# Optimization experiments

Measured on AMD Instinct MI355X. Metric: run time of the kernel, lower is better.

## Reference

```python
import jax, jax.numpy as jnp
import numpy as np

N_GRAPHS = 16
NPG = 420               # nodes per graph (fc1 expects 420*64 flatten)
N = N_GRAPHS * NPG      # 6720
DEG = 8
E = N * DEG             # 53760
HEADS = 4
IN_DIM = 2048
C1 = 1024               # per-head channels, layer 1
C2 = 64                 # layer 2 channels
OUT_DIM = 18
SLOPE = 0.2             # GATConv leaky_relu negative_slope


def _seg_softmax(scores, idx, n):
    # numerically-stable softmax over edges grouped by destination node
    m = jax.lax.stop_gradient(jax.ops.segment_max(scores, idx, num_segments=n))
    ex = jnp.exp(scores - m[idx])
    den = jax.ops.segment_sum(ex, idx, num_segments=n)
    return ex / (den[idx] + 1e-16)


def _transformer_conv(x, src, dst, wq, bq, wk, bk, wv, bv, ws, bs, heads, ch):
    # PyG TransformerConv defaults: concat=True, beta=False, root_weight=True, dropout=0
    n = x.shape[0]
    q = (x @ wq + bq).reshape(n, heads, ch)
    k = (x @ wk + bk).reshape(n, heads, ch)
    v = (x @ wv + bv).reshape(n, heads, ch)
    alpha = jnp.einsum('ehc,ehc->eh', q[dst], k[src]) / (ch ** 0.5)  # [E,H]
    alpha = _seg_softmax(alpha, dst, n)
    out = jax.ops.segment_sum(v[src] * alpha[..., None], dst, num_segments=n)  # [N,H,C]
    return out.reshape(n, heads * ch) + (x @ ws + bs)  # skip connection (lin_skip)


def _gat_conv(x, src, dst, w, a_src, a_dst, bias, heads, ch, concat):
    # PyG GATConv defaults: add_self_loops=True, negative_slope=0.2, lin has no bias
    n = x.shape[0]
    loop = jnp.arange(n, dtype=src.dtype)
    s = jnp.concatenate([src, loop])
    d = jnp.concatenate([dst, loop])
    h = (x @ w).reshape(n, heads, ch)
    es = jnp.einsum('nhc,hc->nh', h, a_src)
    ed = jnp.einsum('nhc,hc->nh', h, a_dst)
    e = jax.nn.leaky_relu(es[s] + ed[d], SLOPE)  # [E+N, H]
    alpha = _seg_softmax(e, d, n)
    out = jax.ops.segment_sum(h[s] * alpha[..., None], d, num_segments=n)  # [N,H,C]
    out = out.reshape(n, heads * ch) if concat else out.mean(axis=1)
    return out + bias


def setup_inputs() -> dict:
    key = jax.random.key(0)
    it = iter(jax.random.split(key, 64))
    def nrm(shape, scale):
        return jax.random.normal(next(it), shape, jnp.float32) * scale
    def lin(fi, fo):
        return nrm((fi, fo), float(1.0 / np.sqrt(fi)))
    p = {}
    p['x'] = nrm((N, IN_DIM), 1.0)
    p['edge_index'] = jax.random.randint(next(it), (2, E), 0, N, dtype=jnp.int32)
    for nm in ['t1_wq', 't1_wk', 't1_wv', 't1_ws']:
        p[nm] = lin(IN_DIM, HEADS * C1)
    for nm in ['t1_bq', 't1_bk', 't1_bv', 't1_bs']:
        p[nm] = jnp.zeros((HEADS * C1,), jnp.float32)
    # TransformerConv 2: 4096 -> 64, 1 head
    for nm in ['t2_wq', 't2_wk', 't2_wv', 't2_ws']:
        p[nm] = lin(HEADS * C1, C2)
    for nm in ['t2_bq', 't2_bk', 't2_bv', 't2_bs']:
        p[nm] = jnp.zeros((C2,), jnp.float32)
    p['g1_w'] = lin(IN_DIM, HEADS * C1)
    p['g1_as'] = nrm((HEADS, C1), 0.02)
    p['g1_ad'] = nrm((HEADS, C1), 0.02)
    p['g1_b'] = jnp.zeros((HEADS * C1,), jnp.float32)
    # GATConv 2: 4096 -> 64, 1 head, concat=False (mean)
    p['g2_w'] = lin(HEADS * C1, C2)
    p['g2_as'] = nrm((1, C2), 0.02)
    p['g2_ad'] = nrm((1, C2), 0.02)
    p['g2_b'] = jnp.zeros((C2,), jnp.float32)
    # MLP head
    p['fc1_w'] = lin(NPG * C2, 256); p['fc1_b'] = jnp.zeros((256,), jnp.float32)
    p['fc2_w'] = lin(256, 128);      p['fc2_b'] = jnp.zeros((128,), jnp.float32)
    p['fc3_w'] = lin(128, 64);       p['fc3_b'] = jnp.zeros((64,), jnp.float32)
    p['fc4_w'] = lin(64, OUT_DIM);   p['fc4_b'] = jnp.zeros((OUT_DIM,), jnp.float32)
    return p


def _forward(edge_index, x,
             t1_wq, t1_bq, t1_wk, t1_bk, t1_wv, t1_bv, t1_ws, t1_bs,
             t2_wq, t2_bq, t2_wk, t2_bk, t2_wv, t2_bv, t2_ws, t2_bs,
             g1_w, g1_as, g1_ad, g1_b, g2_w, g2_as, g2_ad, g2_b,
             fc1_w, fc1_b, fc2_w, fc2_b, fc3_w, fc3_b, fc4_w, fc4_b):
    src, dst = edge_index[0], edge_index[1]
    h = jax.nn.relu(_transformer_conv(x, src, dst, t1_wq, t1_bq, t1_wk, t1_bk,
                                      t1_wv, t1_bv, t1_ws, t1_bs, HEADS, C1))
    h = jax.nn.relu(_transformer_conv(h, src, dst, t2_wq, t2_bq, t2_wk, t2_bk,
                                      t2_wv, t2_bv, t2_ws, t2_bs, 1, C2))
    z = jax.nn.relu(_gat_conv(x, src, dst, g1_w, g1_as, g1_ad, g1_b, HEADS, C1, True))
    z = jax.nn.relu(_gat_conv(z, src, dst, g2_w, g2_as, g2_ad, g2_b, 1, C2, False))
    s = (h + z).reshape(-1, NPG * C2)          # [n_graphs, 26880]
    s = jax.nn.relu(s @ fc1_w + fc1_b)          # dropout = identity at eval
    s = jax.nn.relu(s @ fc2_w + fc2_b)
    s = jax.nn.relu(s @ fc3_w + fc3_b)
    return s @ fc4_w + fc4_b                    # [n_graphs, OUT_DIM]


def reference(x, edge_index,
              t1_wq, t1_bq, t1_wk, t1_bk, t1_wv, t1_bv, t1_ws, t1_bs,
              t2_wq, t2_bq, t2_wk, t2_bk, t2_wv, t2_bv, t2_ws, t2_bs,
              g1_w, g1_as, g1_ad, g1_b, g2_w, g2_as, g2_ad, g2_b,
              fc1_w, fc1_b, fc2_w, fc2_b, fc3_w, fc3_b, fc4_w, fc4_b):
    return _forward(edge_index, x,
                    t1_wq, t1_bq, t1_wk, t1_bk, t1_wv, t1_bv, t1_ws, t1_bs,
                    t2_wq, t2_bq, t2_wk, t2_bk, t2_wv, t2_bv, t2_ws, t2_bs,
                    g1_w, g1_as, g1_ad, g1_b, g2_w, g2_as, g2_ad, g2_b,
                    fc1_w, fc1_b, fc2_w, fc2_b, fc3_w, fc3_b, fc4_w, fc4_b)
```

## Files before the change

kernel.cpp:

```cpp
#include <hip/hip_runtime.h>
#include <stdint.h>
#include <stdio.h>

#define NNODES 6720
#define NEDGES 53760
#define NGRAPH 16
#define INDIM  2048
#define HEADS1 4
#define C1DIM  1024
#define D1     4096
#define C2DIM  64
#define N2     320
#define OUTDIM 18

typedef unsigned short u16;
typedef unsigned int   u32;

__device__ __forceinline__ float b2f(u16 u) {
  union { float f; u32 u; } v; v.u = ((u32)u) << 16; return v.f;
}
__device__ __forceinline__ u16 f2b(float f) {
  union { float f; u32 u; } v; v.f = f;
  u32 r = v.u + 0x7FFFu + ((v.u >> 16) & 1u);
  return (u16)(r >> 16);
}
__device__ __forceinline__ float ldf(const void* p, long i, int isf) {
  return isf ? ((const float*)p)[i] : b2f(((const u16*)p)[i]);
}

typedef __attribute__((ext_vector_type(8))) short bf16x8;
typedef __attribute__((ext_vector_type(4))) float f32x4;

__device__ __forceinline__ void gld_lds16(const u16* g, u16* l) {
  __builtin_amdgcn_global_load_lds((const __attribute__((address_space(1))) void*)g,
                                   (__attribute__((address_space(3))) void*)l, 16, 0, 0);
}

__global__ void detect_dtype(const u16* __restrict__ x, int* flag) {
  __shared__ int cnt;
  if (threadIdx.x == 0) cnt = 0;
  __syncthreads();
  int c = 0;
  for (int i = threadIdx.x; i < 4096; i += 256) {
    u16 u = x[2 * i];
    int e = (u >> 7) & 0xFF;
    if (e >= 118 && e <= 135) c++;
  }
  atomicAdd(&cnt, c);
  __syncthreads();
  if (threadIdx.x == 0) *flag = (cnt > 2048) ? 0 : 1;
}

__global__ void conv_any(const void* __restrict__ src, u16* __restrict__ dst,
                         long n, const int* __restrict__ flag) {
  long i = (long)blockIdx.x * 256 + threadIdx.x;
  long stride = (long)gridDim.x * 256;
  int isf = *flag;
  if (isf) {
    const float* s = (const float*)src;
    for (long j = i; j < n; j += stride) dst[j] = f2b(s[j]);
  } else {
    const u16* s = (const u16*)src;
    for (long j = i; j < n; j += stride) dst[j] = s[j];
  }
}

#define NSMALL 13
struct SmallConv {
  const void* src[NSMALL];
  u16*        dst[NSMALL];
  int         n[NSMALL];
};
__global__ void conv_small(SmallConv sc, const int* __restrict__ flag) {
  int b = blockIdx.x;
  int isf = *flag;
  const void* s = sc.src[b];
  u16* d = sc.dst[b];
  int n = sc.n[b];
  if (isf) {
    const float* sf = (const float*)s;
    for (int i = threadIdx.x; i < n; i += 256) d[i] = f2b(sf[i]);
  } else {
    const u16* sb = (const u16*)s;
    for (int i = threadIdx.x; i < n; i += 256) d[i] = sb[i];
  }
}

__global__ __launch_bounds__(256) void transpose_any(const void* __restrict__ src,
                                                     u16* __restrict__ dst,
                                                     int K, int Ncols,
                                                     const int* __restrict__ flag) {
  __shared__ u16 tile[32][33];
  int isf = *flag;
  int tx = threadIdx.x & 31, ty = threadIdx.x >> 5;
  int c0 = blockIdx.x * 32, r0 = blockIdx.y * 32;
  if (isf) {
    const float* s = (const float*)src;
    #pragma unroll
    for (int i = 0; i < 32; i += 8)
      tile[ty + i][tx] = f2b(s[(long)(r0 + ty + i) * Ncols + c0 + tx]);
  } else {
    const u16* s = (const u16*)src;
    #pragma unroll
    for (int i = 0; i < 32; i += 8)
      tile[ty + i][tx] = s[(long)(r0 + ty + i) * Ncols + c0 + tx];
  }
  __syncthreads();
  #pragma unroll
  for (int i = 0; i < 32; i += 8)
    dst[(long)(c0 + ty + i) * K + r0 + tx] = tile[tx][ty + i];
}

__global__ void pack_bias(const void* bq1, const void* bk1, const void* bv1, const void* bs1,
                          const void* bq2, const void* bk2, const void* bv2, const void* bs2,
                          float* bias1, float* bias2, const int* flag) {
  int isf = *flag;
  int i = blockIdx.x * 256 + threadIdx.x;
  if (i < 20480) {
    float v = 0.f;
    if (i < 4096) v = ldf(bq1, i, isf);
    else if (i < 8192)  v = ldf(bk1, i - 4096, isf);
    else if (i < 12288) v = ldf(bv1, i - 8192, isf);
    else if (i < 16384) v = ldf(bs1, i - 12288, isf);
    bias1[i] = v;
  } else if (i < 20480 + N2) {
    int j = i - 20480; float v = 0.f;
    if (j < 64) v = ldf(bq2, j, isf);
    else if (j < 128) v = ldf(bk2, j - 64, isf);
    else if (j < 192) v = ldf(bv2, j - 128, isf);
    else if (j < 256) v = ldf(bs2, j - 192, isf);
    bias2[j] = v;
  }
}

__global__ __launch_bounds__(256) void gemm_bt_r3(const u16* __restrict__ A,
                                                  const u16* __restrict__ BT,
                                                  const float* __restrict__ bias,
                                                  u16* __restrict__ C,
                                                  int M, int N, int K) {
  __shared__ u16 As[3][128 * 32];
  __shared__ u16 Bs[3][128 * 32];

  const int tid = threadIdx.x, lane = tid & 63, wave = tid >> 6;
  const int m0 = blockIdx.y * 128, n0 = blockIdx.x * 128;
  const int wm = (wave >> 1) * 64, wn = (wave & 1) * 64;

  const int srow = tid >> 2, scp = tid & 3;
  const int scl8 = (scp ^ ((srow >> 1) & 3)) * 8;
  int ar0 = m0 + srow;      if (ar0 >= M) ar0 = M - 1;
  int ar1 = m0 + srow + 64; if (ar1 >= M) ar1 = M - 1;
  const u16* ag0 = A + (long)ar0 * K + scl8;
  const u16* ag1 = A + (long)ar1 * K + scl8;
  const u16* bg0 = BT + (long)(n0 + srow) * K + scl8;
  const u16* bg1 = BT + (long)(n0 + srow + 64) * K + scl8;

  f32x4 acc[4][4];
  #pragma unroll
  for (int i = 0; i < 4; i++)
    #pragma unroll
    for (int j = 0; j < 4; j++) { f32x4 z = {0.f, 0.f, 0.f, 0.f}; acc[i][j] = z; }

  const int fr = lane & 15, q = lane >> 4;
  const int fq = (q ^ ((fr >> 1) & 3)) * 8;
  const int aoff = (wm + fr) * 32 + fq;
  const int boff = (wn + fr) * 32 + fq;

  const int NT = K >> 5;

  auto STAGE = [&](int t, int b) {
    const long k0 = (long)t * 32;
    gld_lds16(ag0 + k0, &As[b][(size_t)tid * 8]);
    gld_lds16(ag1 + k0, &As[b][2048 + (size_t)tid * 8]);
    gld_lds16(bg0 + k0, &Bs[b][(size_t)tid * 8]);
    gld_lds16(bg1 + k0, &Bs[b][2048 + (size_t)tid * 8]);
  };

  STAGE(0, 0); STAGE(1, 1);

  int cur = 0, nxt = 2;
  for (int t = 0; t < NT; ++t) {
    if (t < NT - 1) {
      asm volatile("s_waitcnt vmcnt(4)\n\ts_barrier" ::: "memory");
    } else {
      asm volatile("s_waitcnt vmcnt(0)\n\ts_barrier" ::: "memory");
    }
    if (t + 2 < NT) STAGE(t + 2, nxt);

    const u16* ab = &As[cur][0];
    const u16* bb = &Bs[cur][0];
    bf16x8 af[4], bfv[4];
    #pragma unroll
    for (int i = 0; i < 4; i++) af[i]  = *(const bf16x8*)(ab + aoff + i * 512);
    #pragma unroll
    for (int j = 0; j < 4; j++) bfv[j] = *(const bf16x8*)(bb + boff + j * 512);

    #pragma unroll
    for (int i = 0; i < 4; i++)
      #pragma unroll
      for (int j = 0; j < 4; j++)
        acc[i][j] = __builtin_amdgcn_mfma_f32_16x16x32_bf16(af[i], bfv[j], acc[i][j], 0, 0, 0);

    cur = (cur == 2) ? 0 : cur + 1;
    nxt = (nxt == 2) ? 0 : nxt + 1;
  }

  const int q4 = (lane >> 4) * 4, cl = lane & 15;
  #pragma unroll
  for (int i = 0; i < 4; i++)
    #pragma unroll
    for (int r = 0; r < 4; r++) {
      int row = m0 + wm + i * 16 + q4 + r;
      if (row < M) {
        #pragma unroll
        for (int j = 0; j < 4; j++) {
          int col = n0 + wn + j * 16 + cl;
          C[(long)row * N + col] = f2b(acc[i][j][r] + bias[col]);
        }
      }
    }
}

__global__ __launch_bounds__(256) void gemm2_64(const u16* __restrict__ h1,
                                                const u16* __restrict__ z1,
                                                const u16* __restrict__ wt2,
                                                const float* __restrict__ bias2,
                                                u16* __restrict__ y2) {
  __shared__ u16 As[64 * 64];
  __shared__ u16 Bs[64 * 64];
  const int nt = blockIdx.x;
  const u16* A = (nt < 4) ? h1 : z1;
  const u16* BT = wt2 + (size_t)nt * 64 * D1;
  const int m0 = blockIdx.y * 64, n0 = nt * 64;
  const int tid = threadIdx.x, lane = tid & 63, wave = tid >> 6;

  const int sr = tid >> 3, cp = tid & 7;
  const int cgl8 = (cp ^ (sr & 7)) * 8;
  const u16* ag0 = A + (long)(m0 + sr) * D1 + cgl8;
  const u16* ag1 = ag0 + (long)32 * D1;
  const u16* bg0 = BT + (long)sr * D1 + cgl8;
  const u16* bg1 = bg0 + (long)32 * D1;
  u16* al0 = As + tid * 8;  u16* al1 = As + 2048 + tid * 8;
  u16* bl0 = Bs + tid * 8;  u16* bl1 = Bs + 2048 + tid * 8;

  f32x4 acc[4];
  #pragma unroll
  for (int j = 0; j < 4; j++) { f32x4 z = {0.f, 0.f, 0.f, 0.f}; acc[j] = z; }

  const int fr = lane & 15, q = lane >> 4;
  const int x0 = ((q)     ^ (fr & 7)) * 8;
  const int x1 = ((4 + q) ^ (fr & 7)) * 8;
  const u16* apA = As + (wave * 16 + fr) * 64;

  for (int k0 = 0; k0 < D1; k0 += 64) {
    __syncthreads();
    gld_lds16(ag0 + k0, al0);
    gld_lds16(ag1 + k0, al1);
    gld_lds16(bg0 + k0, bl0);
    gld_lds16(bg1 + k0, bl1);
    __syncthreads();
    bf16x8 a0 = *(const bf16x8*)(apA + x0);
    bf16x8 a1 = *(const bf16x8*)(apA + x1);
    #pragma unroll
    for (int j = 0; j < 4; j++) {
      bf16x8 b0 = *(const bf16x8*)(Bs + (j * 16 + fr) * 64 + x0);
      acc[j] = __builtin_amdgcn_mfma_f32_16x16x32_bf16(a0, b0, acc[j], 0, 0, 0);
    }
    #pragma unroll
    for (int j = 0; j < 4; j++) {
      bf16x8 b1 = *(const bf16x8*)(Bs + (j * 16 + fr) * 64 + x1);
      acc[j] = __builtin_amdgcn_mfma_f32_16x16x32_bf16(a1, b1, acc[j], 0, 0, 0);
    }
  }
  const int q4 = (lane >> 4) * 4, cl = lane & 15;
  #pragma unroll
  for (int j = 0; j < 4; j++)
    #pragma unroll
    for (int r = 0; r < 4; r++) {
      int row = m0 + wave * 16 + q4 + r;
      int col = n0 + j * 16 + cl;
      y2[(long)row * N2 + col] = f2b(acc[j][r] + bias2[col]);
    }
}

__global__ void zero_kernel(int* deg, float* f1sum) {
  int i = blockIdx.x * 256 + threadIdx.x;
  if (i < NNODES) deg[i] = 0;
  if (i < NGRAPH * 256) f1sum[i] = 0.f;
}

__global__ void count_deg(const int* __restrict__ ei, int* deg) {
  int e = blockIdx.x * 256 + threadIdx.x;
  if (e < NEDGES) atomicAdd(&deg[ei[NEDGES + e]], 1);
}

__global__ __launch_bounds__(1024) void scan_deg(const int* __restrict__ deg, int* off, int* cur) {
  __shared__ int sh[1024];
  const int t = threadIdx.x;
  const int PER = 7;
  int base = t * PER;
  int loc[PER];
  int sum = 0;
  #pragma unroll
  for (int i = 0; i < PER; i++) {
    int v = (base + i < NNODES) ? deg[base + i] : 0;
    loc[i] = sum; sum += v;
  }
  sh[t] = sum;
  __syncthreads();
  for (int d = 1; d < 1024; d <<= 1) {
    int v = (t >= d) ? sh[t - d] : 0;
    __syncthreads();
    sh[t] += v;
    __syncthreads();
  }
  int prev = (t > 0) ? sh[t - 1] : 0;
  #pragma unroll
  for (int i = 0; i < PER; i++) {
    int idx = base + i;
    if (idx <= NNODES) {
      int v = prev + loc[i];
      off[idx] = v;
      if (idx < NNODES) cur[idx] = v;
    }
  }
}

__global__ void scatter_edges(const int* __restrict__ ei, int* cur,
                              int* esrc, int* edst) {
  int e = blockIdx.x * 256 + threadIdx.x;
  if (e < NEDGES) {
    int s = ei[e], d = ei[NEDGES + e];
    int p = atomicAdd(&cur[d], 1);
    esrc[p] = s; edst[p] = d;
  }
}

__global__ __launch_bounds__(256) void t1_score_csr(const u16* __restrict__ yqk,
                                                    const int* __restrict__ off,
                                                    const int* __restrict__ esrc,
                                                    float* __restrict__ sc) {
  __shared__ float qsh[4096];
  int n = blockIdx.x, tid = threadIdx.x, lane = tid & 63, wave = tid >> 6;
  const u16* qr = yqk + (long)n * 8192;
  for (int i = tid * 8; i < 4096; i += 2048) {
    uint4 qa = *(const uint4*)(qr + i);
    const u16* qs = (const u16*)&qa;
    #pragma unroll
    for (int j = 0; j < 8; j++) qsh[i + j] = b2f(qs[j]);
  }
  __syncthreads();
  int p0 = off[n], p1 = off[n + 1];
  for (int p = p0 + wave; p < p1; p += 4) {
    const u16* k = yqk + (long)esrc[p] * 8192 + 4096;
    float dot[HEADS1];
    #pragma unroll
    for (int h = 0; h < HEADS1; h++) dot[h] = 0.f;
    #pragma unroll
    for (int h = 0; h < HEADS1; h++) {
      #pragma unroll
      for (int c = 0; c < 2; c++) {
        int idx = h * C1DIM + c * 512 + lane * 8;
        uint4 ka = *(const uint4*)(k + idx);
        const u16* ks = (const u16*)&ka;
        #pragma unroll
        for (int i = 0; i < 8; i++) dot[h] += qsh[idx + i] * b2f(ks[i]);
      }
    }
    #pragma unroll
    for (int h = 0; h < HEADS1; h++) {
      float v = dot[h];
      #pragma unroll
      for (int o = 32; o > 0; o >>= 1) v += __shfl_xor(v, o, 64);
      if (lane == 0) sc[(long)p * HEADS1 + h] = v * (1.0f / 32.0f);
    }
  }
}

__global__ void seg_softmax(const int* __restrict__ off, float* __restrict__ sc,
                            float* __restrict__ selfsc, int heads, int useSelf) {
  int i = blockIdx.x * 256 + threadIdx.x;
  if (i >= NNODES * heads) return;
  int n = i / heads, h = i - n * heads;
  int p0 = off[n], p1 = off[n + 1];
  float m = -3.4e38f;
  for (int p = p0; p < p1; p++) m = fmaxf(m, sc[p * heads + h]);
  if (useSelf) m = fmaxf(m, selfsc[i]);
  float den = 0.f;
  for (int p = p0; p < p1; p++) {
    float e = __expf(sc[p * heads + h] - m);
    sc[p * heads + h] = e; den += e;
  }
  float selfe = 0.f;
  if (useSelf) { selfe = __expf(selfsc[i] - m); den += selfe; }
  float inv = 1.0f / (den + 1e-16f);
  for (int p = p0; p < p1; p++) sc[p * heads + h] *= inv;
  if (useSelf) selfsc[i] = selfe * inv;
}

__global__ __launch_bounds__(256) void t1_agg(const u16* __restrict__ yvs,
                                              const int* __restrict__ off,
                                              const int* __restrict__ esrc,
                                              const float* __restrict__ alpha,
                                              u16* __restrict__ h1) {
  int n = blockIdx.x, t = threadIdx.x, h = t >> 6;
  int p0 = off[n], p1 = off[n + 1];
  float acc[16];
  #pragma unroll
  for (int i = 0; i < 16; i++) acc[i] = 0.f;
  for (int p = p0; p < p1; p++) {
    float a = alpha[p * 4 + h];
    const u16* v = yvs + (long)esrc[p] * 8192 + t * 16;
    uint4 v0 = *(const uint4*)(v);
    uint4 v1 = *(const uint4*)(v + 8);
    const u16* s0 = (const u16*)&v0; const u16* s1 = (const u16*)&v1;
    #pragma unroll
    for (int i = 0; i < 8; i++) acc[i] += a * b2f(s0[i]);
    #pragma unroll
    for (int i = 0; i < 8; i++) acc[8 + i] += a * b2f(s1[i]);
  }
  const u16* sk = yvs + (long)n * 8192 + 4096 + t * 16;
  uint4 k0 = *(const uint4*)(sk); uint4 k1 = *(const uint4*)(sk + 8);
  const u16* ks0 = (const u16*)&k0; const u16* ks1 = (const u16*)&k1;
  u16 outv[16];
  #pragma unroll
  for (int i = 0; i < 8; i++) outv[i] = f2b(fmaxf(acc[i] + b2f(ks0[i]), 0.f));
  #pragma unroll
  for (int i = 0; i < 8; i++) outv[8 + i] = f2b(fmaxf(acc[8 + i] + b2f(ks1[i]), 0.f));
  *(uint4*)(h1 + (long)n * D1 + t * 16) = *(uint4*)outv;
  *(uint4*)(h1 + (long)n * D1 + t * 16 + 8) = *(uint4*)(outv + 8);
}

__global__ __launch_bounds__(256) void g1_dots(const u16* __restrict__ gat,
                                               const u16* __restrict__ a_src,
                                               const u16* __restrict__ a_dst,
                                               float* __restrict__ es, float* __restrict__ ed) {
  int n = blockIdx.x;
  int h = threadIdx.x >> 6, lane = threadIdx.x & 63;
  const u16* hr = gat + (long)n * D1 + h * C1DIM;
  const u16* as = a_src + h * C1DIM;
  const u16* ad = a_dst + h * C1DIM;
  float s1 = 0.f, s2 = 0.f;
  #pragma unroll
  for (int c = 0; c < 2; c++) {
    int idx = c * 512 + lane * 8;
    uint4 hv = *(const uint4*)(hr + idx);
    uint4 av = *(const uint4*)(as + idx);
    uint4 dv = *(const uint4*)(ad + idx);
    const u16* hs = (const u16*)&hv; const u16* a1 = (const u16*)&av; const u16* d1 = (const u16*)&dv;
    #pragma unroll
    for (int i = 0; i < 8; i++) {
      float x = b2f(hs[i]);
      s1 += x * b2f(a1[i]); s2 += x * b2f(d1[i]);
    }
  }
  #pragma unroll
  for (int o = 32; o > 0; o >>= 1) { s1 += __shfl_xor(s1, o, 64); s2 += __shfl_xor(s2, o, 64); }
  if (lane == 0) { es[n * 4 + h] = s1; ed[n * 4 + h] = s2; }
}

__global__ void gat_score(const int* __restrict__ esrc, const int* __restrict__ edst,
                          const float* __restrict__ es, const float* __restrict__ ed,
                          float* __restrict__ sc, float* __restrict__ selfsc, int heads) {
  int i = blockIdx.x * 256 + threadIdx.x;
  int ne = NEDGES * heads;
  if (i < ne) {
    int p = i / heads, h = i - p * heads;
    float v = es[esrc[p] * heads + h] + ed[edst[p] * heads + h];
    sc[i] = (v > 0.f) ? v : 0.2f * v;
  } else {
    int j = i - ne;
    if (j < NNODES * heads) {
      float v = es[j] + ed[j];
      selfsc[j] = (v > 0.f) ? v : 0.2f * v;
    }
  }
}

__global__ __launch_bounds__(256) void g1_agg(const u16* __restrict__ gat,
                                              const int* __restrict__ off,
                                              const int* __restrict__ esrc,
                                              const float* __restrict__ alpha,
                                              const float* __restrict__ selfa,
                                              const u16* __restrict__ bias,
                                              u16* __restrict__ z1) {
  int n = blockIdx.x, t = threadIdx.x, h = t >> 6;
  int p0 = off[n], p1 = off[n + 1];
  float acc[16];
  #pragma unroll
  for (int i = 0; i < 16; i++) acc[i] = 0.f;
  for (int p = p0; p < p1; p++) {
    float a = alpha[p * 4 + h];
    const u16* v = gat + (long)esrc[p] * D1 + t * 16;
    uint4 v0 = *(const uint4*)(v);
    uint4 v1 = *(const uint4*)(v + 8);
    const u16* s0 = (const u16*)&v0; const u16* s1 = (const u16*)&v1;
    #pragma unroll
    for (int i = 0; i < 8; i++) acc[i] += a * b2f(s0[i]);
    #pragma unroll
    for (int i = 0; i < 8; i++) acc[8 + i] += a * b2f(s1[i]);
  }
  {
    float a = selfa[n * 4 + h];
    const u16* v = gat + (long)n * D1 + t * 16;
    uint4 v0 = *(const uint4*)(v);
    uint4 v1 = *(const uint4*)(v + 8);
    const u16* s0 = (const u16*)&v0; const u16* s1 = (const u16*)&v1;
    #pragma unroll
    for (int i = 0; i < 8; i++) acc[i] += a * b2f(s0[i]);
    #pragma unroll
    for (int i = 0; i < 8; i++) acc[8 + i] += a * b2f(s1[i]);
  }
  u16 outv[16];
  #pragma unroll
  for (int i = 0; i < 16; i++) outv[i] = f2b(fmaxf(acc[i] + b2f(bias[t * 16 + i]), 0.f));
  *(uint4*)(z1 + (long)n * D1 + t * 16) = *(uint4*)outv;
  *(uint4*)(z1 + (long)n * D1 + t * 16 + 8) = *(uint4*)(outv + 8);
}

__global__ __launch_bounds__(256) void t2_score(const u16* __restrict__ y2,
                                                const int* __restrict__ esrc,
                                                const int* __restrict__ edst,
                                                float* __restrict__ sc) {
  int w = (blockIdx.x * 256 + threadIdx.x) >> 6, lane = threadIdx.x & 63;
  if (w >= NEDGES) return;
  float q = b2f(y2[(long)edst[w] * N2 + lane]);
  float k = b2f(y2[(long)esrc[w] * N2 + C2DIM + lane]);
  float v = q * k;
  #pragma unroll
  for (int o = 32; o > 0; o >>= 1) v += __shfl_xor(v, o, 64);
  if (lane == 0) sc[w] = v * 0.125f;
}

__global__ __launch_bounds__(256) void t2_agg(const u16* __restrict__ y2,
                                              const int* __restrict__ off,
                                              const int* __restrict__ esrc,
                                              const float* __restrict__ alpha,
                                              float* __restrict__ sn) {
  int n = (blockIdx.x * 256 + threadIdx.x) >> 6, lane = threadIdx.x & 63;
  if (n >= NNODES) return;
  int p0 = off[n], p1 = off[n + 1];
  float acc = 0.f;
  for (int p = p0; p < p1; p++)
    acc += alpha[p] * b2f(y2[(long)esrc[p] * N2 + 2 * C2DIM + lane]);
  acc += b2f(y2[(long)n * N2 + 3 * C2DIM + lane]);
  sn[(long)n * C2DIM + lane] = fmaxf(acc, 0.f);
}

__global__ __launch_bounds__(256) void g2_dots(const u16* __restrict__ y2,
                                               const u16* __restrict__ as,
                                               const u16* __restrict__ ad,
                                               float* __restrict__ es, float* __restrict__ ed) {
  int n = (blockIdx.x * 256 + threadIdx.x) >> 6, lane = threadIdx.x & 63;
  if (n >= NNODES) return;
  float x = b2f(y2[(long)n * N2 + 4 * C2DIM + lane]);
  float s1 = x * b2f(as[lane]), s2 = x * b2f(ad[lane]);
  #pragma unroll
  for (int o = 32; o > 0; o >>= 1) { s1 += __shfl_xor(s1, o, 64); s2 += __shfl_xor(s2, o, 64); }
  if (lane == 0) { es[n] = s1; ed[n] = s2; }
}

__global__ __launch_bounds__(256) void g2_agg(const u16* __restrict__ y2,
                                              const int* __restrict__ off,
                                              const int* __restrict__ esrc,
                                              const float* __restrict__ alpha,
                                              const float* __restrict__ selfa,
                                              const u16* __restrict__ bias,
                                              float* __restrict__ sn) {
  int n = (blockIdx.x * 256 + threadIdx.x) >> 6, lane = threadIdx.x & 63;
  if (n >= NNODES) return;
  int p0 = off[n], p1 = off[n + 1];
  float acc = 0.f;
  for (int p = p0; p < p1; p++)
    acc += alpha[p] * b2f(y2[(long)esrc[p] * N2 + 4 * C2DIM + lane]);
  acc += selfa[n] * b2f(y2[(long)n * N2 + 4 * C2DIM + lane]);
  float v = fmaxf(acc + b2f(bias[lane]), 0.f);
  sn[(long)n * C2DIM + lane] += v;
}

#define FCHUNK 210
__global__ __launch_bounds__(256) void fc1_partial(const float* __restrict__ sn,
                                                   const void* __restrict__ w,
                                                   const int* __restrict__ flag,
                                                   float* __restrict__ f1sum) {
  __shared__ float sl[16 * FCHUNK];
  int k0 = blockIdx.x * FCHUNK;
  int t = threadIdx.x;
  int isf = *flag;
  for (int idx = t; idx < 16 * FCHUNK; idx += 256) {
    int g = idx / FCHUNK, kk = idx - g * FCHUNK;
    sl[idx] = sn[(long)g * 26880 + k0 + kk];
  }
  __syncthreads();
  float acc[16];
  #pragma unroll
  for (int g = 0; g < 16; g++) acc[g] = 0.f;
  if (isf) {
    const float* wf = (const float*)w;
    for (int kk = 0; kk < FCHUNK; kk++) {
      float wv = wf[(long)(k0 + kk) * 256 + t];
      #pragma unroll
      for (int g = 0; g < 16; g++) acc[g] += sl[g * FCHUNK + kk] * wv;
    }
  } else {
    const u16* wb = (const u16*)w;
    for (int kk = 0; kk < FCHUNK; kk++) {
      float wv = b2f(wb[(long)(k0 + kk) * 256 + t]);
      #pragma unroll
      for (int g = 0; g < 16; g++) acc[g] += sl[g * FCHUNK + kk] * wv;
    }
  }
  #pragma unroll
  for (int g = 0; g < 16; g++) atomicAdd(&f1sum[g * 256 + t], acc[g]);
}

__global__ __launch_bounds__(256) void fc_tail(const float* __restrict__ f1sum,
                                               const u16* b1, const u16* w2, const u16* b2,
                                               const u16* w3, const u16* b3,
                                               const u16* w4, const u16* b4,
                                               void* __restrict__ out,
                                               const int* __restrict__ flag) {
  __shared__ float A1[16 * 256];
  __shared__ float A2[16 * 128];
  __shared__ float A3[16 * 64];
  int isf = *flag;
  int t = threadIdx.x;
  for (int i = t; i < 4096; i += 256) A1[i] = fmaxf(f1sum[i] + b2f(b1[i & 255]), 0.f);
  __syncthreads();
  for (int i = t; i < 2048; i += 256) {
    int g = i >> 7, j = i & 127;
    float acc = b2f(b2[j]);
    for (int k = 0; k < 256; k++) acc += A1[g * 256 + k] * b2f(w2[k * 128 + j]);
    A2[i] = fmaxf(acc, 0.f);
  }
  __syncthreads();
  for (int i = t; i < 1024; i += 256) {
    int g = i >> 6, j = i & 63;
    float acc = b2f(b3[j]);
    for (int k = 0; k < 128; k++) acc += A2[g * 128 + k] * b2f(w3[k * 64 + j]);
    A3[i] = fmaxf(acc, 0.f);
  }
  __syncthreads();
  for (int i = t; i < NGRAPH * OUTDIM; i += 256) {
    int g = i / OUTDIM, j = i - g * OUTDIM;
    float acc = b2f(b4[j]);
    for (int k = 0; k < 64; k++) acc += A3[g * 64 + k] * b2f(w4[k * OUTDIM + j]);
    if (isf) ((float*)out)[i] = acc;
    else     ((u16*)out)[i] = f2b(acc);
  }
}

extern "C" void kernel_launch(void* const* d_in, const int* in_sizes, int n_in,
                              void* d_out, int out_size, void* d_ws, size_t ws_size,
                              hipStream_t stream) {
  const void* x     = d_in[0];
  const int*  ei    = (const int*)d_in[1];
  const void* t1_wq = d_in[2];
  const void* t1_wk = d_in[3];
  const void* t1_wv = d_in[4];
  const void* t1_ws = d_in[5];
  const void* t1_bq = d_in[6];
  const void* t1_bk = d_in[7];
  const void* t1_bv = d_in[8];
  const void* t1_bs = d_in[9];
  const void* t2_wq = d_in[10];
  const void* t2_wk = d_in[11];
  const void* t2_wv = d_in[12];
  const void* t2_ws = d_in[13];
  const void* t2_bq = d_in[14];
  const void* t2_bk = d_in[15];
  const void* t2_bv = d_in[16];
  const void* t2_bs = d_in[17];
  const void* g1_w  = d_in[18];
  const void* g1_as = d_in[19];
  const void* g1_ad = d_in[20];
  const void* g1_b  = d_in[21];
  const void* g2_w  = d_in[22];
  const void* g2_as = d_in[23];
  const void* g2_ad = d_in[24];
  const void* g2_b  = d_in[25];
  const void* fc1_w = d_in[26];
  const void* fc1_b = d_in[27];
  const void* fc2_w = d_in[28];
  const void* fc2_b = d_in[29];
  const void* fc3_w = d_in[30];
  const void* fc3_b = d_in[31];
  const void* fc4_w = d_in[32];
  const void* fc4_b = d_in[33];

  char* wp = (char*)d_ws;
  auto alloc = [&](size_t bytes) {
    char* p = wp; wp += (bytes + 255) & ~(size_t)255; return p;
  };
  u16*   wtSlab = (u16*)  alloc((size_t)8192 * INDIM * 2);
  u16*   wt2    = (u16*)  alloc((size_t)N2 * D1 * 2);
  u16*   yqk    = (u16*)  alloc((size_t)NNODES * 8192 * 2);
  u16*   h1     = (u16*)  alloc((size_t)NNODES * D1 * 2);
  u16*   y2     = (u16*)  alloc((size_t)NNODES * N2 * 2);
  u16*   xb     = (u16*)  alloc((size_t)NNODES * INDIM * 2);
  u16*   fc2wb  = (u16*)  alloc((size_t)256 * 128 * 2);
  u16*   fc3wb  = (u16*)  alloc((size_t)128 * 64 * 2);
  u16*   fc4wb  = (u16*)  alloc((size_t)64 * OUTDIM * 2);
  u16*   fb1    = (u16*)  alloc(256 * 2);
  u16*   fb2    = (u16*)  alloc(128 * 2);
  u16*   fb3    = (u16*)  alloc(64 * 2);
  u16*   fb4    = (u16*)  alloc(OUTDIM * 2);
  u16*   g1asb  = (u16*)  alloc(4096 * 2);
  u16*   g1adb  = (u16*)  alloc(4096 * 2);
  u16*   g1bb   = (u16*)  alloc(4096 * 2);
  u16*   g2asb  = (u16*)  alloc(64 * 2);
  u16*   g2adb  = (u16*)  alloc(64 * 2);
  u16*   g2bb   = (u16*)  alloc(64 * 2);
  float* bias1  = (float*)alloc((size_t)20480 * 4);
  float* bias2  = (float*)alloc((size_t)N2 * 4);
  int*   flag   = (int*)  alloc(256);
  int*   deg    = (int*)  alloc((size_t)NNODES * 4);
  int*   off    = (int*)  alloc((size_t)(NNODES + 1) * 4);
  int*   cur    = (int*)  alloc((size_t)NNODES * 4);
  int*   esrc   = (int*)  alloc((size_t)NEDGES * 4);
  int*   edst   = (int*)  alloc((size_t)NEDGES * 4);
  float* scT1   = (float*)alloc((size_t)NEDGES * 4 * 4);
  float* esG1   = (float*)alloc((size_t)NNODES * 4 * 4);
  float* edG1   = (float*)alloc((size_t)NNODES * 4 * 4);
  float* scG1   = (float*)alloc((size_t)NEDGES * 4 * 4);
  float* sfG1   = (float*)alloc((size_t)NNODES * 4 * 4);
  float* scT2   = (float*)alloc((size_t)NEDGES * 4);
  float* scG2   = (float*)alloc((size_t)NEDGES * 4);
  float* sfG2   = (float*)alloc((size_t)NNODES * 4);
  float* es2    = (float*)alloc((size_t)NNODES * 4);
  float* ed2    = (float*)alloc((size_t)NNODES * 4);
  float* sn     = (float*)alloc((size_t)NNODES * C2DIM * 4);
  float* f1sum  = (float*)alloc((size_t)NGRAPH * 256 * 4);

  u16* gat = yqk;
  u16* z1  = yqk + (size_t)NNODES * D1;

  size_t need = (size_t)(wp - (char*)d_ws);
  if (ws_size < need) {
    fprintf(stderr, "[GATGT kernel] WORKSPACE TOO SMALL ws=%zu need=%zu\n", ws_size, need);
    return;
  }

  detect_dtype<<<1, 256, 0, stream>>>((const u16*)x, flag);

  zero_kernel<<<27, 256, 0, stream>>>(deg, f1sum);
  count_deg<<<NEDGES / 256, 256, 0, stream>>>(ei, deg);
  scan_deg<<<1, 1024, 0, stream>>>(deg, off, cur);
  scatter_edges<<<NEDGES / 256, 256, 0, stream>>>(ei, cur, esrc, edst);
  pack_bias<<<82, 256, 0, stream>>>(t1_bq, t1_bk, t1_bv, t1_bs,
                                    t2_bq, t2_bk, t2_bv, t2_bs, bias1, bias2, flag);

  conv_any<<<4096, 256, 0, stream>>>(x, xb, (long)NNODES * INDIM, flag);
  {
    SmallConv sc;
    const void* srcs[NSMALL] = { fc2_w, fc3_w, fc4_w, fc1_b, fc2_b, fc3_b, fc4_b,
                                 g1_as, g1_ad, g1_b, g2_as, g2_ad, g2_b };
    u16* dsts[NSMALL] = { fc2wb, fc3wb, fc4wb, fb1, fb2, fb3, fb4,
                          g1asb, g1adb, g1bb, g2asb, g2adb, g2bb };
    int  ns[NSMALL]   = { 256 * 128, 128 * 64, 64 * OUTDIM, 256, 128, 64, OUTDIM,
                          4096, 4096, 4096, 64, 64, 64 };
    for (int i = 0; i < NSMALL; i++) { sc.src[i] = srcs[i]; sc.dst[i] = dsts[i]; sc.n[i] = ns[i]; }
    conv_small<<<NSMALL, 256, 0, stream>>>(sc, flag);
  }

  transpose_any<<<dim3(128, 64), 256, 0, stream>>>(t1_wq, wtSlab, INDIM, 4096, flag);
  transpose_any<<<dim3(128, 64), 256, 0, stream>>>(t1_wk, wtSlab + (size_t)4096 * INDIM, INDIM, 4096, flag);
  gemm_bt_r3<<<dim3(64, 53), 256, 0, stream>>>(xb, wtSlab, bias1, yqk, NNODES, 8192, INDIM);
  t1_score_csr<<<NNODES, 256, 0, stream>>>(yqk, off, esrc, scT1);
  seg_softmax<<<105, 256, 0, stream>>>(off, scT1, nullptr, 4, 0);

  transpose_any<<<dim3(128, 64), 256, 0, stream>>>(t1_wv, wtSlab, INDIM, 4096, flag);
  transpose_any<<<dim3(128, 64), 256, 0, stream>>>(t1_ws, wtSlab + (size_t)4096 * INDIM, INDIM, 4096, flag);
  gemm_bt_r3<<<dim3(64, 53), 256, 0, stream>>>(xb, wtSlab, bias1 + 8192, yqk, NNODES, 8192, INDIM);
  t1_agg<<<NNODES, 256, 0, stream>>>(yqk, off, esrc, scT1, h1);

  transpose_any<<<dim3(128, 64), 256, 0, stream>>>(g1_w, wtSlab, INDIM, 4096, flag);
  gemm_bt_r3<<<dim3(32, 53), 256, 0, stream>>>(xb, wtSlab, bias1 + 16384, gat, NNODES, 4096, INDIM);
  g1_dots<<<NNODES, 256, 0, stream>>>(gat, g1asb, g1adb, esG1, edG1);
  gat_score<<<(NEDGES * 4 + NNODES * 4 + 255) / 256, 256, 0, stream>>>(
      esrc, edst, esG1, edG1, scG1, sfG1, 4);
  seg_softmax<<<105, 256, 0, stream>>>(off, scG1, sfG1, 4, 1);
  g1_agg<<<NNODES, 256, 0, stream>>>(gat, off, esrc, scG1, sfG1, g1bb, z1);

  {
    const void* srcs2[5] = { t2_wq, t2_wk, t2_wv, t2_ws, g2_w };
    for (int s = 0; s < 5; s++)
      transpose_any<<<dim3(2, 128), 256, 0, stream>>>(
          srcs2[s], wt2 + (size_t)s * 64 * D1, D1, 64, flag);
  }
  gemm2_64<<<dim3(5, NNODES / 64), 256, 0, stream>>>(h1, z1, wt2, bias2, y2);

  t2_score<<<NEDGES / 4, 256, 0, stream>>>(y2, esrc, edst, scT2);
  seg_softmax<<<(NNODES + 255) / 256, 256, 0, stream>>>(off, scT2, nullptr, 1, 0);
  t2_agg<<<NNODES / 4, 256, 0, stream>>>(y2, off, esrc, scT2, sn);

  g2_dots<<<NNODES / 4, 256, 0, stream>>>(y2, g2asb, g2adb, es2, ed2);
  gat_score<<<(NEDGES + NNODES + 255) / 256, 256, 0, stream>>>(
      esrc, edst, es2, ed2, scG2, sfG2, 1);
  seg_softmax<<<(NNODES + 255) / 256, 256, 0, stream>>>(off, scG2, sfG2, 1, 1);
  g2_agg<<<NNODES / 4, 256, 0, stream>>>(y2, off, esrc, scG2, sfG2, g2bb, sn);

  fc1_partial<<<128, 256, 0, stream>>>(sn, fc1_w, flag, f1sum);
  fc_tail<<<1, 256, 0, stream>>>(f1sum, fb1, fc2wb, fb2, fc3wb, fb3,
                                 fc4wb, fb4, d_out, flag);
}
```

Measured before the change: 1.527 ms.

## Fuse edge scoring with segment softmax per node and merge layer-2 kernels

Edge-score kernels now also run the destination-node softmax in shared memory, one block per node, so the separate one-thread-per-(node,head) seg_softmax launches go away. Nodes whose in-degree exceeds a cap fall back to a serial path. Layer 2 computes the GAT source and destination dots in the GEMM epilogue, scores both attention types in one kernel, and aggregates both in one pass over each neighbour row. The aim is fewer launches and fewer global round-trips for the score arrays, at the cost of launching many small one-block-per-node grids.

```diff
diff --git a/kernel.cpp b/kernel.cpp
--- a/kernel.cpp
+++ b/kernel.cpp
@@ -12,6 +12,7 @@
 #define C2DIM  64
 #define N2     320
 #define OUTDIM 18
+#define SMCAP  256
 
 typedef unsigned short u16;
 typedef unsigned int   u32;
@@ -224,7 +225,11 @@
                                                 const u16* __restrict__ z1,
                                                 const u16* __restrict__ wt2,
                                                 const float* __restrict__ bias2,
-                                                u16* __restrict__ y2) {
+                                                const u16* __restrict__ as64,
+                                                const u16* __restrict__ ad64,
+                                                u16* __restrict__ y2,
+                                                float* __restrict__ es2,
+                                                float* __restrict__ ed2) {
   __shared__ u16 As[64 * 64];
   __shared__ u16 Bs[64 * 64];
   const int nt = blockIdx.x;
@@ -280,6 +285,26 @@
       int col = n0 + j * 16 + cl;
       y2[(long)row * N2 + col] = f2b(acc[j][r] + bias2[col]);
     }
+  if (nt == 4) {
+    #pragma unroll
+    for (int r = 0; r < 4; r++) {
+      int row = m0 + wave * 16 + q4 + r;
+      float s1 = 0.f, s2 = 0.f;
+      #pragma unroll
+      for (int j = 0; j < 4; j++) {
+        int col = j * 16 + cl;
+        float v = b2f(f2b(acc[j][r] + bias2[256 + col]));
+        s1 += v * b2f(as64[col]);
+        s2 += v * b2f(ad64[col]);
+      }
+      #pragma unroll
+      for (int o = 1; o < 16; o <<= 1) {
+        s1 += __shfl_xor(s1, o, 64);
+        s2 += __shfl_xor(s2, o, 64);
+      }
+      if (cl == 0) { es2[row] = s1; ed2[row] = s2; }
+    }
+  }
 }
 
 __global__ void zero_kernel(int* deg, float* f1sum) {
@@ -335,11 +360,12 @@
   }
 }
 
-__global__ __launch_bounds__(256) void t1_score_csr(const u16* __restrict__ yqk,
-                                                    const int* __restrict__ off,
-                                                    const int* __restrict__ esrc,
-                                                    float* __restrict__ sc) {
+__global__ __launch_bounds__(256) void t1_score_sm(const u16* __restrict__ yqk,
+                                                   const int* __restrict__ off,
+                                                   const int* __restrict__ esrc,
+                                                   float* __restrict__ sc) {
   __shared__ float qsh[4096];
+  __shared__ float sm[SMCAP * 4];
   int n = blockIdx.x, tid = threadIdx.x, lane = tid & 63, wave = tid >> 6;
   const u16* qr = yqk + (long)n * 8192;
   for (int i = tid * 8; i < 4096; i += 2048) {
@@ -349,7 +375,8 @@
     for (int j = 0; j < 8; j++) qsh[i + j] = b2f(qs[j]);
   }
   __syncthreads();
-  int p0 = off[n], p1 = off[n + 1];
+  int p0 = off[n], p1 = off[n + 1], deg = p1 - p0;
+  bool fits = (deg <= SMCAP);
   for (int p = p0 + wave; p < p1; p += 4) {
     const u16* k = yqk + (long)esrc[p] * 8192 + 4096;
     float dot[HEADS1];
@@ -371,30 +398,42 @@
       float v = dot[h];
       #pragma unroll
       for (int o = 32; o > 0; o >>= 1) v += __shfl_xor(v, o, 64);
-      if (lane == 0) sc[(long)p * HEADS1 + h] = v * (1.0f / 32.0f);
-    }
-  }
-}
-
-__global__ void seg_softmax(const int* __restrict__ off, float* __restrict__ sc,
-                            float* __restrict__ selfsc, int heads, int useSelf) {
-  int i = blockIdx.x * 256 + threadIdx.x;
-  if (i >= NNODES * heads) return;
-  int n = i / heads, h = i - n * heads;
-  int p0 = off[n], p1 = off[n + 1];
-  float m = -3.4e38f;
-  for (int p = p0; p < p1; p++) m = fmaxf(m, sc[p * heads + h]);
-  if (useSelf) m = fmaxf(m, selfsc[i]);
-  float den = 0.f;
-  for (int p = p0; p < p1; p++) {
-    float e = __expf(sc[p * heads + h] - m);
-    sc[p * heads + h] = e; den += e;
-  }
-  float selfe = 0.f;
-  if (useSelf) { selfe = __expf(selfsc[i] - m); den += selfe; }
-  float inv = 1.0f / (den + 1e-16f);
-  for (int p = p0; p < p1; p++) sc[p * heads + h] *= inv;
-  if (useSelf) selfsc[i] = selfe * inv;
+      if (lane == 0) {
+        float sv = v * (1.0f / 32.0f);
+        if (fits) sm[(p - p0) * 4 + h] = sv;
+        else      sc[(long)p * HEADS1 + h] = sv;
+      }
+    }
+  }
+  __syncthreads();
+  if (fits) {
+    int h = wave;
+    float m = -3.4e38f;
+    for (int e = lane; e < deg; e += 64) m = fmaxf(m, sm[e * 4 + h]);
+    #pragma unroll
+    for (int o = 32; o > 0; o >>= 1) m = fmaxf(m, __shfl_xor(m, o, 64));
+    float s = 0.f;
+    for (int e = lane; e < deg; e += 64) {
+      float ex = __expf(sm[e * 4 + h] - m);
+      sm[e * 4 + h] = ex; s += ex;
+    }
+    #pragma unroll
+    for (int o = 32; o > 0; o >>= 1) s += __shfl_xor(s, o, 64);
+    float inv = 1.0f / (s + 1e-16f);
+    for (int e = lane; e < deg; e += 64)
+      sc[(long)(p0 + e) * 4 + h] = sm[e * 4 + h] * inv;
+  } else if (tid < 4) {
+    int h = tid;
+    float m = -3.4e38f;
+    for (int p = p0; p < p1; p++) m = fmaxf(m, sc[(long)p * 4 + h]);
+    float s = 0.f;
+    for (int p = p0; p < p1; p++) {
+      float ex = __expf(sc[(long)p * 4 + h] - m);
+      sc[(long)p * 4 + h] = ex; s += ex;
+    }
+    float inv = 1.0f / (s + 1e-16f);
+    for (int p = p0; p < p1; p++) sc[(long)p * 4 + h] *= inv;
+  }
 }
 
 __global__ __launch_bounds__(256) void t1_agg(const u16* __restrict__ yvs,
@@ -458,21 +497,59 @@
   if (lane == 0) { es[n * 4 + h] = s1; ed[n * 4 + h] = s2; }
 }
 
-__global__ void gat_score(const int* __restrict__ esrc, const int* __restrict__ edst,
-                          const float* __restrict__ es, const float* __restrict__ ed,
-                          float* __restrict__ sc, float* __restrict__ selfsc, int heads) {
-  int i = blockIdx.x * 256 + threadIdx.x;
-  int ne = NEDGES * heads;
-  if (i < ne) {
-    int p = i / heads, h = i - p * heads;
-    float v = es[esrc[p] * heads + h] + ed[edst[p] * heads + h];
-    sc[i] = (v > 0.f) ? v : 0.2f * v;
-  } else {
-    int j = i - ne;
-    if (j < NNODES * heads) {
-      float v = es[j] + ed[j];
-      selfsc[j] = (v > 0.f) ? v : 0.2f * v;
-    }
+__global__ __launch_bounds__(256) void g1_score_sm(const int* __restrict__ off,
+                                                   const int* __restrict__ esrc,
+                                                   const float* __restrict__ es,
+                                                   const float* __restrict__ ed,
+                                                   float* __restrict__ sc,
+                                                   float* __restrict__ selfsc) {
+  __shared__ float sm[SMCAP * 4];
+  int n = blockIdx.x, tid = threadIdx.x, lane = tid & 63, wave = tid >> 6;
+  int p0 = off[n], p1 = off[n + 1], deg = p1 - p0;
+  bool fits = (deg <= SMCAP);
+  for (int idx = tid; idx < deg * 4; idx += 256) {
+    int e = idx >> 2, h = idx & 3;
+    float v = es[esrc[p0 + e] * 4 + h] + ed[n * 4 + h];
+    v = (v > 0.f) ? v : 0.2f * v;
+    if (fits) sm[idx] = v;
+    else      sc[(long)(p0 + e) * 4 + h] = v;
+  }
+  __syncthreads();
+  if (fits) {
+    int h = wave;
+    float sv = es[n * 4 + h] + ed[n * 4 + h];
+    sv = (sv > 0.f) ? sv : 0.2f * sv;
+    float m = sv;
+    for (int e = lane; e < deg; e += 64) m = fmaxf(m, sm[e * 4 + h]);
+    #pragma unroll
+    for (int o = 32; o > 0; o >>= 1) m = fmaxf(m, __shfl_xor(m, o, 64));
+    float s = 0.f;
+    for (int e = lane; e < deg; e += 64) {
+      float ex = __expf(sm[e * 4 + h] - m);
+      sm[e * 4 + h] = ex; s += ex;
+    }
+    #pragma unroll
+    for (int o = 32; o > 0; o >>= 1) s += __shfl_xor(s, o, 64);
+    float selfe = __expf(sv - m);
+    float inv = 1.0f / (s + selfe + 1e-16f);
+    for (int e = lane; e < deg; e += 64)
+      sc[(long)(p0 + e) * 4 + h] = sm[e * 4 + h] * inv;
+    if (lane == 0) selfsc[n * 4 + h] = selfe * inv;
+  } else if (tid < 4) {
+    int h = tid;
+    float sv = es[n * 4 + h] + ed[n * 4 + h];
+    sv = (sv > 0.f) ? sv : 0.2f * sv;
+    float m = sv;
+    for (int p = p0; p < p1; p++) m = fmaxf(m, sc[(long)p * 4 + h]);
+    float s = 0.f;
+    for (int p = p0; p < p1; p++) {
+      float ex = __expf(sc[(long)p * 4 + h] - m);
+      sc[(long)p * 4 + h] = ex; s += ex;
+    }
+    float selfe = __expf(sv - m);
+    float inv = 1.0f / (s + selfe + 1e-16f);
+    for (int p = p0; p < p1; p++) sc[(long)p * 4 + h] *= inv;
+    selfsc[n * 4 + h] = selfe * inv;
   }
 }
 
@@ -517,64 +594,107 @@
   *(uint4*)(z1 + (long)n * D1 + t * 16 + 8) = *(uint4*)(outv + 8);
 }
 
-__global__ __launch_bounds__(256) void t2_score(const u16* __restrict__ y2,
-                                                const int* __restrict__ esrc,
-                                                const int* __restrict__ edst,
-                                                float* __restrict__ sc) {
-  int w = (blockIdx.x * 256 + threadIdx.x) >> 6, lane = threadIdx.x & 63;
-  if (w >= NEDGES) return;
-  float q = b2f(y2[(long)edst[w] * N2 + lane]);
-  float k = b2f(y2[(long)esrc[w] * N2 + C2DIM + lane]);
-  float v = q * k;
-  #pragma unroll
-  for (int o = 32; o > 0; o >>= 1) v += __shfl_xor(v, o, 64);
-  if (lane == 0) sc[w] = v * 0.125f;
-}
-
-__global__ __launch_bounds__(256) void t2_agg(const u16* __restrict__ y2,
-                                              const int* __restrict__ off,
-                                              const int* __restrict__ esrc,
-                                              const float* __restrict__ alpha,
-                                              float* __restrict__ sn) {
+__global__ __launch_bounds__(256) void t2g2_score_sm(const u16* __restrict__ y2,
+                                                     const int* __restrict__ off,
+                                                     const int* __restrict__ esrc,
+                                                     const float* __restrict__ es2,
+                                                     const float* __restrict__ ed2,
+                                                     float* __restrict__ scT,
+                                                     float* __restrict__ scG,
+                                                     float* __restrict__ sfG) {
+  __shared__ float smT[SMCAP];
+  __shared__ float smG[SMCAP];
+  int n = blockIdx.x, tid = threadIdx.x, lane = tid & 63, wave = tid >> 6;
+  int p0 = off[n], p1 = off[n + 1], deg = p1 - p0;
+  bool fits = (deg <= SMCAP);
+  float qv = b2f(y2[(long)n * N2 + lane]);
+  float edn = ed2[n];
+  for (int e = wave; e < deg; e += 4) {
+    int s = esrc[p0 + e];
+    float kv = b2f(y2[(long)s * N2 + C2DIM + lane]);
+    float d = qv * kv;
+    #pragma unroll
+    for (int o = 32; o > 0; o >>= 1) d += __shfl_xor(d, o, 64);
+    if (lane == 0) {
+      float vt = d * 0.125f;
+      float vg = es2[s] + edn;
+      vg = (vg > 0.f) ? vg : 0.2f * vg;
+      if (fits) { smT[e] = vt; smG[e] = vg; }
+      else      { scT[p0 + e] = vt; scG[p0 + e] = vg; }
+    }
+  }
+  __syncthreads();
+  if (fits) {
+    if (wave == 0) {
+      float m = -3.4e38f;
+      for (int e = lane; e < deg; e += 64) m = fmaxf(m, smT[e]);
+      #pragma unroll
+      for (int o = 32; o > 0; o >>= 1) m = fmaxf(m, __shfl_xor(m, o, 64));
+      float s = 0.f;
+      for (int e = lane; e < deg; e += 64) { float ex = __expf(smT[e] - m); smT[e] = ex; s += ex; }
+      #pragma unroll
+      for (int o = 32; o > 0; o >>= 1) s += __shfl_xor(s, o, 64);
+      float inv = 1.0f / (s + 1e-16f);
+      for (int e = lane; e < deg; e += 64) scT[p0 + e] = smT[e] * inv;
+    } else if (wave == 1) {
+      float sv = es2[n] + edn;
+      sv = (sv > 0.f) ? sv : 0.2f * sv;
+      float m = sv;
+      for (int e = lane; e < deg; e += 64) m = fmaxf(m, smG[e]);
+      #pragma unroll
+      for (int o = 32; o > 0; o >>= 1) m = fmaxf(m, __shfl_xor(m, o, 64));
+      float s = 0.f;
+      for (int e = lane; e < deg; e += 64) { float ex = __expf(smG[e] - m); smG[e] = ex; s += ex; }
+      #pragma unroll
+      for (int o = 32; o > 0; o >>= 1) s += __shfl_xor(s, o, 64);
+      float selfe = __expf(sv - m);
+      float inv = 1.0f / (s + selfe + 1e-16f);
+      for (int e = lane; e < deg; e += 64) scG[p0 + e] = smG[e] * inv;
+      if (lane == 0) sfG[n] = selfe * inv;
+    }
+  } else {
+    if (tid == 0) {
+      float m = -3.4e38f;
+      for (int p = p0; p < p1; p++) m = fmaxf(m, scT[p]);
+      float s = 0.f;
+      for (int p = p0; p < p1; p++) { float ex = __expf(scT[p] - m); scT[p] = ex; s += ex; }
+      float inv = 1.0f / (s + 1e-16f);
+      for (int p = p0; p < p1; p++) scT[p] *= inv;
+    } else if (tid == 1) {
+      float sv = es2[n] + edn;
+      sv = (sv > 0.f) ? sv : 0.2f * sv;
+      float m = sv;
+      for (int p = p0; p < p1; p++) m = fmaxf(m, scG[p]);
+      float s = 0.f;
+      for (int p = p0; p < p1; p++) { float ex = __expf(scG[p] - m); scG[p] = ex; s += ex; }
+      float selfe = __expf(sv - m);
+      float inv = 1.0f / (s + selfe + 1e-16f);
+      for (int p = p0; p < p1; p++) scG[p] *= inv;
+      sfG[n] = selfe * inv;
+    }
+  }
+}
+
+__global__ __launch_bounds__(256) void tg2_agg(const u16* __restrict__ y2,
+                                               const int* __restrict__ off,
+                                               const int* __restrict__ esrc,
+                                               const float* __restrict__ alphaT,
+                                               const float* __restrict__ alphaG,
+                                               const float* __restrict__ selfaG,
+                                               const u16* __restrict__ bias,
+                                               float* __restrict__ sn) {
   int n = (blockIdx.x * 256 + threadIdx.x) >> 6, lane = threadIdx.x & 63;
   if (n >= NNODES) return;
   int p0 = off[n], p1 = off[n + 1];
-  float acc = 0.f;
-  for (int p = p0; p < p1; p++)
-    acc += alpha[p] * b2f(y2[(long)esrc[p] * N2 + 2 * C2DIM + lane]);
-  acc += b2f(y2[(long)n * N2 + 3 * C2DIM + lane]);
-  sn[(long)n * C2DIM + lane] = fmaxf(acc, 0.f);
-}
-
-__global__ __launch_bounds__(256) void g2_dots(const u16* __restrict__ y2,
-                                               const u16* __restrict__ as,
-                                               const u16* __restrict__ ad,
-                                               float* __restrict__ es, float* __restrict__ ed) {
-  int n = (blockIdx.x * 256 + threadIdx.x) >> 6, lane = threadIdx.x & 63;
-  if (n >= NNODES) return;
-  float x = b2f(y2[(long)n * N2 + 4 * C2DIM + lane]);
-  float s1 = x * b2f(as[lane]), s2 = x * b2f(ad[lane]);
-  #pragma unroll
-  for (int o = 32; o > 0; o >>= 1) { s1 += __shfl_xor(s1, o, 64); s2 += __shfl_xor(s2, o, 64); }
-  if (lane == 0) { es[n] = s1; ed[n] = s2; }
-}
-
-__global__ __launch_bounds__(256) void g2_agg(const u16* __restrict__ y2,
-                                              const int* __restrict__ off,
-                                              const int* __restrict__ esrc,
-                                              const float* __restrict__ alpha,
-                                              const float* __restrict__ selfa,
-                                              const u16* __restrict__ bias,
-                                              float* __restrict__ sn) {
-  int n = (blockIdx.x * 256 + threadIdx.x) >> 6, lane = threadIdx.x & 63;
-  if (n >= NNODES) return;
-  int p0 = off[n], p1 = off[n + 1];
-  float acc = 0.f;
-  for (int p = p0; p < p1; p++)
-    acc += alpha[p] * b2f(y2[(long)esrc[p] * N2 + 4 * C2DIM + lane]);
-  acc += selfa[n] * b2f(y2[(long)n * N2 + 4 * C2DIM + lane]);
-  float v = fmaxf(acc + b2f(bias[lane]), 0.f);
-  sn[(long)n * C2DIM + lane] += v;
+  float at = 0.f, ag = 0.f;
+  for (int p = p0; p < p1; p++) {
+    const u16* row = y2 + (long)esrc[p] * N2;
+    at += alphaT[p] * b2f(row[2 * C2DIM + lane]);
+    ag += alphaG[p] * b2f(row[4 * C2DIM + lane]);
+  }
+  at += b2f(y2[(long)n * N2 + 3 * C2DIM + lane]);
+  ag += selfaG[n] * b2f(y2[(long)n * N2 + 4 * C2DIM + lane]);
+  sn[(long)n * C2DIM + lane] = fmaxf(at, 0.f) + fmaxf(ag + b2f(bias[lane]), 0.f);
 }
 
 #define FCHUNK 210
@@ -765,8 +885,7 @@
   transpose_any<<<dim3(128, 64), 256, 0, stream>>>(t1_wq, wtSlab, INDIM, 4096, flag);
   transpose_any<<<dim3(128, 64), 256, 0, stream>>>(t1_wk, wtSlab + (size_t)4096 * INDIM, INDIM, 4096, flag);
   gemm_bt_r3<<<dim3(64, 53), 256, 0, stream>>>(xb, wtSlab, bias1, yqk, NNODES, 8192, INDIM);
-  t1_score_csr<<<NNODES, 256, 0, stream>>>(yqk, off, esrc, scT1);
-  seg_softmax<<<105, 256, 0, stream>>>(off, scT1, nullptr, 4, 0);
+  t1_score_sm<<<NNODES, 256, 0, stream>>>(yqk, off, esrc, scT1);
 
   transpose_any<<<dim3(128, 64), 256, 0, stream>>>(t1_wv, wtSlab, INDIM, 4096, flag);
   transpose_any<<<dim3(128, 64), 256, 0, stream>>>(t1_ws, wtSlab + (size_t)4096 * INDIM, INDIM, 4096, flag);
@@ -776,9 +895,7 @@
   transpose_any<<<dim3(128, 64), 256, 0, stream>>>(g1_w, wtSlab, INDIM, 4096, flag);
   gemm_bt_r3<<<dim3(32, 53), 256, 0, stream>>>(xb, wtSlab, bias1 + 16384, gat, NNODES, 4096, INDIM);
   g1_dots<<<NNODES, 256, 0, stream>>>(gat, g1asb, g1adb, esG1, edG1);
-  gat_score<<<(NEDGES * 4 + NNODES * 4 + 255) / 256, 256, 0, stream>>>(
-      esrc, edst, esG1, edG1, scG1, sfG1, 4);
-  seg_softmax<<<105, 256, 0, stream>>>(off, scG1, sfG1, 4, 1);
+  g1_score_sm<<<NNODES, 256, 0, stream>>>(off, esrc, esG1, edG1, scG1, sfG1);
   g1_agg<<<NNODES, 256, 0, stream>>>(gat, off, esrc, scG1, sfG1, g1bb, z1);
 
   {
@@ -787,17 +904,11 @@
       transpose_any<<<dim3(2, 128), 256, 0, stream>>>(
           srcs2[s], wt2 + (size_t)s * 64 * D1, D1, 64, flag);
   }
-  gemm2_64<<<dim3(5, NNODES / 64), 256, 0, stream>>>(h1, z1, wt2, bias2, y2);
-
-  t2_score<<<NEDGES / 4, 256, 0, stream>>>(y2, esrc, edst, scT2);
-  seg_softmax<<<(NNODES + 255) / 256, 256, 0, stream>>>(off, scT2, nullptr, 1, 0);
-  t2_agg<<<NNODES / 4, 256, 0, stream>>>(y2, off, esrc, scT2, sn);
-
-  g2_dots<<<NNODES / 4, 256, 0, stream>>>(y2, g2asb, g2adb, es2, ed2);
-  gat_score<<<(NEDGES + NNODES + 255) / 256, 256, 0, stream>>>(
-      esrc, edst, es2, ed2, scG2, sfG2, 1);
-  seg_softmax<<<(NNODES + 255) / 256, 256, 0, stream>>>(off, scG2, sfG2, 1, 1);
-  g2_agg<<<NNODES / 4, 256, 0, stream>>>(y2, off, esrc, scG2, sfG2, g2bb, sn);
+  gemm2_64<<<dim3(5, NNODES / 64), 256, 0, stream>>>(h1, z1, wt2, bias2,
+                                                     g2asb, g2adb, y2, es2, ed2);
+
+  t2g2_score_sm<<<NNODES, 256, 0, stream>>>(y2, off, esrc, es2, ed2, scT2, scG2, sfG2);
+  tg2_agg<<<NNODES / 4, 256, 0, stream>>>(y2, off, esrc, scT2, scG2, sfG2, g2bb, sn);
 
   fc1_partial<<<128, 256, 0, stream>>>(sn, fc1_w, flag, f1sum);
   fc_tail<<<1, 256, 0, stream>>>(f1sum, fb1, fc2wb, fb2, fc3wb, fb3,
```

Measured after the change: 1.473 ms. 1.04x faster.
